# Kernel optimization log

Hardware: AMD Instinct MI355X
Metric: run time of the kernel (lower is better)

## Reference

```python
import jax, jax.numpy as jnp
import numpy as np

N = 50000      # nodes
K = 15         # k_max candidate neighbors per node
D = 128        # node_dim
H = 64         # hidden_dim
K_MIN = 2.0
K_MAX = 15.0
TAU = 0.5      # edge_tau
LAM = 1.0      # selector_lambda


def setup_inputs() -> dict:
    key = jax.random.key(0)
    ks = jax.random.split(key, 16)
    x = jax.random.normal(ks[0], (N, D), dtype=jnp.float32)
    src = jax.random.randint(ks[1], (N * K,), 0, N)
    dst = jnp.repeat(jnp.arange(N), K)  # edges grouped by dst, as the module requires
    edge_index = jnp.stack([src, dst]).astype(jnp.int64)
    edge_dist = jax.random.uniform(ks[2], (N * K,), dtype=jnp.float32)

    def lin(k, fin, fout):
        return jax.random.normal(k, (fin, fout), dtype=jnp.float32) / np.sqrt(fin)

    EIN = 2 * D + 1  # edge MLP input: [x_dst, x_src, dist]
    return {
        "x": x, "edge_index": edge_index, "edge_dist": edge_dist,
        "ew1": lin(ks[3], EIN, H), "eb1": jnp.zeros((H,), jnp.float32),
        "ew2": lin(ks[4], H, H),   "eb2": jnp.zeros((H,), jnp.float32),
        "ew3": lin(ks[5], H, 1),   "eb3": jnp.zeros((1,), jnp.float32),
        "dw1": lin(ks[6], D + 1, H), "db1": jnp.zeros((H,), jnp.float32),
        "dw2": lin(ks[7], H, H),     "db2": jnp.zeros((H,), jnp.float32),
        "dw3": lin(ks[8], H, 1),     "db3": jnp.zeros((1,), jnp.float32),
    }


def reference(x, edge_index, edge_dist, ew1, eb1, ew2, eb2, ew3, eb3,
              dw1, db1, dw2, db2, dw3, db3):
    src_mat = edge_index[0].reshape(N, K)              # (N, K)
    x_src = x[src_mat]                                 # gather: (N, K, D)
    x_dst = jnp.broadcast_to(x[:, None, :], (N, K, D))
    edge_feat = jnp.concatenate([x_dst, x_src, edge_dist.reshape(N, K, 1)], axis=-1)

    # edge MLP -> logits (eval mode: no gumbel-logistic noise)
    h = jax.nn.relu(edge_feat @ ew1 + eb1)
    h = jax.nn.relu(h @ ew2 + eb2)
    edge_logits = (h @ ew3 + eb3)[..., 0]              # (N, K)
    edge_energy = jax.nn.sigmoid(edge_logits / TAU)

    # degree MLP -> continuous k per node
    degree_hint = edge_energy.sum(axis=1, keepdims=True)
    g = jax.nn.relu(jnp.concatenate([x, degree_hint], axis=1) @ dw1 + db1)
    g = jax.nn.relu(g @ dw2 + db2)
    k_raw = (g @ dw3 + db3)[:, 0]
    k_cont = K_MIN + (K_MAX - K_MIN) * jax.nn.sigmoid(k_raw)  # (N,)

    # per-node descending sort + straight-through top-k gate
    perm = jnp.argsort(-edge_energy, axis=1)
    energy_sorted = jnp.take_along_axis(edge_energy, perm, axis=1)
    ranks = jnp.arange(1, K + 1, dtype=x.dtype)[None, :]
    gate_soft = jax.nn.sigmoid((k_cont[:, None] - ranks) / LAM)
    k_int = jnp.clip(jnp.round(k_cont), K_MIN, K_MAX)
    gate_hard = (ranks <= k_int[:, None]).astype(gate_soft.dtype)
    gate = gate_soft + jax.lax.stop_gradient(gate_hard - gate_soft)

    gated_sorted = energy_sorted * gate
    inv_perm = jnp.argsort(perm, axis=1)               # undo the sort
    edge_gate = jnp.take_along_axis(gate, inv_perm, axis=1)
    edge_weight = jnp.take_along_axis(gated_sorted, inv_perm, axis=1)

    denom = jnp.maximum(edge_weight.sum(axis=1, keepdims=True), 1e-12)
    edge_weight = edge_weight / denom
    return (edge_weight.reshape(-1), edge_gate.reshape(-1),
            edge_energy.reshape(-1), k_cont)
```

## Files before the change

kernel.cpp:

```cpp
#include <hip/hip_runtime.h>
#include <cmath>

#define NN 50000
#define KK 15
#define DD 128
#define HH 64
#define NKE (NN * KK)

__global__ __launch_bounds__(256) void kP(const float* __restrict__ x,
                                          const float* __restrict__ ew1,
                                          const float* __restrict__ dw1,
                                          float* __restrict__ ws) {
    int lane = threadIdx.x & 63;
    int wv = __builtin_amdgcn_readfirstlane((int)(threadIdx.x >> 6));
    int r0 = blockIdx.x * 32 + wv * 8;
    if (r0 >= NN) return;

    const float* W0 = ew1;
    const float* W1 = ew1 + DD * HH;
    const float* W2 = dw1;
    const float* xw = x + (size_t)r0 * DD;

    float a0[8], a1[8], a2[8];
#pragma unroll
    for (int r = 0; r < 8; ++r) { a0[r] = 0.f; a1[r] = 0.f; a2[r] = 0.f; }

#pragma unroll 1
    for (int i4 = 0; i4 < DD / 4; ++i4) {
        float w00 = W0[(i4 * 4 + 0) * HH + lane];
        float w01 = W0[(i4 * 4 + 1) * HH + lane];
        float w02 = W0[(i4 * 4 + 2) * HH + lane];
        float w03 = W0[(i4 * 4 + 3) * HH + lane];
        float w10 = W1[(i4 * 4 + 0) * HH + lane];
        float w11 = W1[(i4 * 4 + 1) * HH + lane];
        float w12 = W1[(i4 * 4 + 2) * HH + lane];
        float w13 = W1[(i4 * 4 + 3) * HH + lane];
        float w20 = W2[(i4 * 4 + 0) * HH + lane];
        float w21 = W2[(i4 * 4 + 1) * HH + lane];
        float w22 = W2[(i4 * 4 + 2) * HH + lane];
        float w23 = W2[(i4 * 4 + 3) * HH + lane];
#pragma unroll
        for (int r = 0; r < 8; ++r) {
            float4 xv = *(const float4*)(xw + r * DD + i4 * 4);
            a0[r] = fmaf(xv.x, w00, a0[r]);
            a0[r] = fmaf(xv.y, w01, a0[r]);
            a0[r] = fmaf(xv.z, w02, a0[r]);
            a0[r] = fmaf(xv.w, w03, a0[r]);
            a1[r] = fmaf(xv.x, w10, a1[r]);
            a1[r] = fmaf(xv.y, w11, a1[r]);
            a1[r] = fmaf(xv.z, w12, a1[r]);
            a1[r] = fmaf(xv.w, w13, a1[r]);
            a2[r] = fmaf(xv.x, w20, a2[r]);
            a2[r] = fmaf(xv.y, w21, a2[r]);
            a2[r] = fmaf(xv.z, w22, a2[r]);
            a2[r] = fmaf(xv.w, w23, a2[r]);
        }
    }
    float* o0 = ws + (size_t)r0 * HH + lane;
    float* o1 = ws + (size_t)NN * HH + (size_t)r0 * HH + lane;
    float* o2 = ws + 2 * (size_t)NN * HH + (size_t)r0 * HH + lane;
#pragma unroll
    for (int r = 0; r < 8; ++r) {
        o0[r * HH] = a0[r];
        o1[r * HH] = a1[r];
        o2[r * HH] = a2[r];
    }
}

__global__ __launch_bounds__(128, 4) void kE(const int* __restrict__ srcIdx,
                                             const float* __restrict__ dist,
                                             const float* __restrict__ ws,
                                             const float* __restrict__ ew1,
                                             const float* __restrict__ eb1,
                                             const float* __restrict__ ew2,
                                             const float* __restrict__ eb2,
                                             const float* __restrict__ ew3,
                                             const float* __restrict__ eb3,
                                             float* __restrict__ energy_out) {
    int lane = threadIdx.x & 63;
    int wv = __builtin_amdgcn_readfirstlane((int)(threadIdx.x >> 6));
    int e = blockIdx.x * 64 + lane;
    __shared__ float lred[2][64];

    bool valid = e < NKE;
    int ec = valid ? e : (NKE - 1);
    int s = srcIdx[ec];
    int d = ec / KK;
    float dd = dist[ec];
    const float* A = ws + (size_t)d * HH;
    const float* B = ws + (size_t)NN * HH + (size_t)s * HH;
    const float* w1l = ew1 + 2 * DD * HH;
    const float* W2  = ew2 + wv * 32;
    const float* eb2s = eb2 + wv * 32;
    const float* ew3s = ew3 + wv * 32;

    float acc[32];
#pragma unroll
    for (int j = 0; j < 32; ++j) acc[j] = 0.f;

    float4 a4 = *(const float4*)A;
    float4 b4 = *(const float4*)B;
#pragma unroll 1
    for (int i4 = 0; i4 < HH / 4; ++i4) {
        float4 a = a4, b = b4;
        int nx = (i4 + 1 < HH / 4) ? (i4 + 1) : i4;
        a4 = *(const float4*)(A + nx * 4);
        b4 = *(const float4*)(B + nx * 4);
        float h[4];
        h[0] = fmaxf(a.x + b.x + dd * w1l[i4 * 4 + 0] + eb1[i4 * 4 + 0], 0.f);
        h[1] = fmaxf(a.y + b.y + dd * w1l[i4 * 4 + 1] + eb1[i4 * 4 + 1], 0.f);
        h[2] = fmaxf(a.z + b.z + dd * w1l[i4 * 4 + 2] + eb1[i4 * 4 + 2], 0.f);
        h[3] = fmaxf(a.w + b.w + dd * w1l[i4 * 4 + 3] + eb1[i4 * 4 + 3], 0.f);
#pragma unroll
        for (int k = 0; k < 4; ++k) {
            const float* wr = W2 + (i4 * 4 + k) * HH;
#pragma unroll
            for (int j4 = 0; j4 < 8; ++j4) {
                float4 w = *(const float4*)(wr + j4 * 4);
                acc[j4 * 4 + 0] = fmaf(h[k], w.x, acc[j4 * 4 + 0]);
                acc[j4 * 4 + 1] = fmaf(h[k], w.y, acc[j4 * 4 + 1]);
                acc[j4 * 4 + 2] = fmaf(h[k], w.z, acc[j4 * 4 + 2]);
                acc[j4 * 4 + 3] = fmaf(h[k], w.w, acc[j4 * 4 + 3]);
            }
        }
    }
    float lg = 0.f;
#pragma unroll
    for (int j = 0; j < 32; ++j)
        lg = fmaf(fmaxf(acc[j] + eb2s[j], 0.f), ew3s[j], lg);

    lred[wv][lane] = lg;
    __syncthreads();
    if (wv == 0 && valid) {
        float t = lred[0][lane] + lred[1][lane] + eb3[0];
        energy_out[e] = 1.f / (1.f + expf(-2.f * t));
    }
}

__global__ __launch_bounds__(256, 2) void kF(const float* __restrict__ ws,
                                             const float* __restrict__ dw1,
                                             const float* __restrict__ db1,
                                             const float* __restrict__ dw2,
                                             const float* __restrict__ db2,
                                             const float* __restrict__ dw3,
                                             const float* __restrict__ db3,
                                             float* __restrict__ out) {
    int lane = threadIdx.x & 63;
    int wv = __builtin_amdgcn_readfirstlane((int)(threadIdx.x >> 6));
    int n = blockIdx.x * 64 + lane;
    __shared__ float kred[4][64];

    bool valid = n < NN;
    int nc = valid ? n : (NN - 1);
    const float* energy = out + 2 * (size_t)NKE;

    float ev[KK];
    float dh = 0.f;
#pragma unroll
    for (int j = 0; j < KK; ++j) {
        ev[j] = energy[(size_t)nc * KK + j];
        dh += ev[j];
    }

    const float* XC  = ws + 2 * (size_t)NN * HH + (size_t)nc * HH;
    const float* w1l = dw1 + DD * HH;
    const float* W2  = dw2 + wv * 16;
    const float* db2s = db2 + wv * 16;
    const float* dw3s = dw3 + wv * 16;

    float acc[16];
#pragma unroll
    for (int j = 0; j < 16; ++j) acc[j] = 0.f;

    float4 c4 = *(const float4*)XC;
#pragma unroll 1
    for (int i4 = 0; i4 < HH / 4; ++i4) {
        float4 c = c4;
        int nx = (i4 + 1 < HH / 4) ? (i4 + 1) : i4;
        c4 = *(const float4*)(XC + nx * 4);
        float cv[4] = {c.x, c.y, c.z, c.w};
#pragma unroll
        for (int m = 0; m < 4; ++m) {
            int k = i4 * 4 + m;
            float g = fmaxf(cv[m] + dh * w1l[k] + db1[k], 0.f);
            const float* wr = W2 + k * HH;
#pragma unroll
            for (int j4 = 0; j4 < 4; ++j4) {
                float4 w = *(const float4*)(wr + j4 * 4);
                acc[j4 * 4 + 0] = fmaf(g, w.x, acc[j4 * 4 + 0]);
                acc[j4 * 4 + 1] = fmaf(g, w.y, acc[j4 * 4 + 1]);
                acc[j4 * 4 + 2] = fmaf(g, w.z, acc[j4 * 4 + 2]);
                acc[j4 * 4 + 3] = fmaf(g, w.w, acc[j4 * 4 + 3]);
            }
        }
    }
    float kp_ = 0.f;
#pragma unroll
    for (int j = 0; j < 16; ++j)
        kp_ = fmaf(fmaxf(acc[j] + db2s[j], 0.f), dw3s[j], kp_);

    kred[wv][lane] = kp_;
    __syncthreads();
    float kraw = kred[0][lane] + kred[1][lane] + kred[2][lane] + kred[3][lane]
               + db3[0];
    if (!valid) return;

    float kcont = 2.f + 13.f / (1.f + expf(-kraw));
    if (wv == 3) out[3 * (size_t)NKE + n] = kcont;

    float se[16];
    int si[16];
#pragma unroll
    for (int j = 0; j < KK; ++j) { se[j] = ev[j]; si[j] = j; }
    se[15] = -1.f; si[15] = 15;

#pragma unroll
    for (int pp = 1; pp < 16; pp <<= 1) {
#pragma unroll
        for (int k = pp; k >= 1; k >>= 1) {
#pragma unroll
            for (int j = k & (pp - 1); j + k < 16; j += 2 * k) {
#pragma unroll
                for (int i = 0; i < k; ++i) {
                    int a = i + j, b = i + j + k;
                    if (b < 16 && (a / (2 * pp)) == (b / (2 * pp))) {
                        bool sw = (se[b] > se[a]) ||
                                  (se[b] == se[a] && si[b] < si[a]);
                        float ea = sw ? se[b] : se[a];
                        float eb = sw ? se[a] : se[b];
                        int ia = sw ? si[b] : si[a];
                        int ib = sw ? si[a] : si[b];
                        se[a] = ea; se[b] = eb; si[a] = ia; si[b] = ib;
                    }
                }
            }
        }
    }

    float kint = rintf(kcont);
    kint = fminf(fmaxf(kint, 2.f), 15.f);

    float wsrt[KK];
    float denom = 0.f;
#pragma unroll
    for (int r = 0; r < KK; ++r) {
        float sel = ((float)(r + 1) <= kint) ? 1.f : 0.f;
        float wvv = se[r] * sel;
        wsrt[r] = wvv;
        denom += wvv;
    }
    denom = fmaxf(denom, 1e-12f);

#pragma unroll
    for (int r = 0; r < KK; ++r) {
        if ((r & 3) == wv) {
            float sel = ((float)(r + 1) <= kint) ? 1.f : 0.f;
            int j0 = si[r];
            out[(size_t)NKE + (size_t)n * KK + j0] = sel;
            out[(size_t)n * KK + j0] = wsrt[r] / denom;
        }
    }
}

extern "C" void kernel_launch(void* const* d_in, const int* in_sizes, int n_in,
                              void* d_out, int out_size, void* d_ws, size_t ws_size,
                              hipStream_t stream) {
    const float* x   = (const float*)d_in[0];
    const int*   ei  = (const int*)d_in[1];
    const float* ed  = (const float*)d_in[2];
    const float* ew1 = (const float*)d_in[3];
    const float* eb1 = (const float*)d_in[4];
    const float* ew2 = (const float*)d_in[5];
    const float* eb2 = (const float*)d_in[6];
    const float* ew3 = (const float*)d_in[7];
    const float* eb3 = (const float*)d_in[8];
    const float* dw1 = (const float*)d_in[9];
    const float* db1 = (const float*)d_in[10];
    const float* dw2 = (const float*)d_in[11];
    const float* db2 = (const float*)d_in[12];
    const float* dw3 = (const float*)d_in[13];
    const float* db3 = (const float*)d_in[14];
    float* out = (float*)d_out;
    float* ws  = (float*)d_ws;

    hipLaunchKernelGGL(kP, dim3((NN + 31) / 32), dim3(256), 0, stream,
                       x, ew1, dw1, ws);
    hipLaunchKernelGGL(kE, dim3((NKE + 63) / 64), dim3(128), 0, stream,
                       ei, ed, ws, ew1, eb1, ew2, eb2, ew3, eb3,
                       out + 2 * (size_t)NKE);
    hipLaunchKernelGGL(kF, dim3((NN + 63) / 64), dim3(256), 0, stream,
                       ws, dw1, db1, dw2, db2, dw3, db3, out);
}
```

Measured before the change: 291.5 us.

## Stage x tiles in LDS for projection and compute full hidden per edge thread

The projection kernel now loads a 64-row tile of x into padded shared memory. Each wave computes 32 output columns for 64 rows, with one row per lane and uniform (scalar/broadcast) weight loads, replacing the previous layout where lanes mapped to output columns. The edge kernel now gives each thread one edge and all 64 hidden units, which removes the two-wave split, the shared-memory reduction and the barrier, and halves the redundant A/B gathers. In exchange the edge kernel holds 64 accumulators per thread, which raises register pressure and may lower occupancy.

```diff
diff --git a/kernel.cpp b/kernel.cpp
--- a/kernel.cpp
+++ b/kernel.cpp
@@ -7,63 +7,61 @@
 #define HH 64
 #define NKE (NN * KK)
 
-__global__ __launch_bounds__(256) void kP(const float* __restrict__ x,
-                                          const float* __restrict__ ew1,
-                                          const float* __restrict__ dw1,
-                                          float* __restrict__ ws) {
-    int lane = threadIdx.x & 63;
-    int wv = __builtin_amdgcn_readfirstlane((int)(threadIdx.x >> 6));
-    int r0 = blockIdx.x * 32 + wv * 8;
-    if (r0 >= NN) return;
-
-    const float* W0 = ew1;
-    const float* W1 = ew1 + DD * HH;
-    const float* W2 = dw1;
-    const float* xw = x + (size_t)r0 * DD;
-
-    float a0[8], a1[8], a2[8];
-#pragma unroll
-    for (int r = 0; r < 8; ++r) { a0[r] = 0.f; a1[r] = 0.f; a2[r] = 0.f; }
-
+#define TP_ROWS 64
+#define TP_STRIDE 129
+
+__global__ __launch_bounds__(384, 2) void kP(const float* __restrict__ x,
+                                             const float* __restrict__ ew1,
+                                             const float* __restrict__ dw1,
+                                             float* __restrict__ ws) {
+    __shared__ float xt[TP_ROWS * TP_STRIDE];
+    int t = threadIdx.x;
+    int lane = t & 63;
+    int w = __builtin_amdgcn_readfirstlane(t >> 6);
+    int seg = w >> 1;
+    int jh  = w & 1;
+    int row0 = blockIdx.x * TP_ROWS;
+
+    for (int i = t; i < TP_ROWS * DD / 4; i += 384) {
+        int r = (i * 4) / DD;
+        int c = (i * 4) % DD;
+        float4 v = make_float4(0.f, 0.f, 0.f, 0.f);
+        if (row0 + r < NN) v = *(const float4*)(x + (size_t)(row0 + r) * DD + c);
+        float* p = &xt[r * TP_STRIDE + c];
+        p[0] = v.x; p[1] = v.y; p[2] = v.z; p[3] = v.w;
+    }
+    __syncthreads();
+
+    const float* Wb = (seg == 0) ? (ew1 + jh * 32)
+                    : (seg == 1) ? (ew1 + (size_t)DD * HH + jh * 32)
+                                 : (dw1 + jh * 32);
+
+    float acc[32];
+#pragma unroll
+    for (int j = 0; j < 32; ++j) acc[j] = 0.f;
+
+    const float* xrow = &xt[lane * TP_STRIDE];
 #pragma unroll 1
-    for (int i4 = 0; i4 < DD / 4; ++i4) {
-        float w00 = W0[(i4 * 4 + 0) * HH + lane];
-        float w01 = W0[(i4 * 4 + 1) * HH + lane];
-        float w02 = W0[(i4 * 4 + 2) * HH + lane];
-        float w03 = W0[(i4 * 4 + 3) * HH + lane];
-        float w10 = W1[(i4 * 4 + 0) * HH + lane];
-        float w11 = W1[(i4 * 4 + 1) * HH + lane];
-        float w12 = W1[(i4 * 4 + 2) * HH + lane];
-        float w13 = W1[(i4 * 4 + 3) * HH + lane];
-        float w20 = W2[(i4 * 4 + 0) * HH + lane];
-        float w21 = W2[(i4 * 4 + 1) * HH + lane];
-        float w22 = W2[(i4 * 4 + 2) * HH + lane];
-        float w23 = W2[(i4 * 4 + 3) * HH + lane];
-#pragma unroll
-        for (int r = 0; r < 8; ++r) {
-            float4 xv = *(const float4*)(xw + r * DD + i4 * 4);
-            a0[r] = fmaf(xv.x, w00, a0[r]);
-            a0[r] = fmaf(xv.y, w01, a0[r]);
-            a0[r] = fmaf(xv.z, w02, a0[r]);
-            a0[r] = fmaf(xv.w, w03, a0[r]);
-            a1[r] = fmaf(xv.x, w10, a1[r]);
-            a1[r] = fmaf(xv.y, w11, a1[r]);
-            a1[r] = fmaf(xv.z, w12, a1[r]);
-            a1[r] = fmaf(xv.w, w13, a1[r]);
-            a2[r] = fmaf(xv.x, w20, a2[r]);
-            a2[r] = fmaf(xv.y, w21, a2[r]);
-            a2[r] = fmaf(xv.z, w22, a2[r]);
-            a2[r] = fmaf(xv.w, w23, a2[r]);
-        }
-    }
-    float* o0 = ws + (size_t)r0 * HH + lane;
-    float* o1 = ws + (size_t)NN * HH + (size_t)r0 * HH + lane;
-    float* o2 = ws + 2 * (size_t)NN * HH + (size_t)r0 * HH + lane;
-#pragma unroll
-    for (int r = 0; r < 8; ++r) {
-        o0[r * HH] = a0[r];
-        o1[r * HH] = a1[r];
-        o2[r * HH] = a2[r];
+    for (int k = 0; k < DD; ++k) {
+        float xv = xrow[k];
+        const float* wr = Wb + (size_t)k * HH;
+#pragma unroll
+        for (int j4 = 0; j4 < 8; ++j4) {
+            float4 wv = *(const float4*)(wr + j4 * 4);
+            acc[j4 * 4 + 0] = fmaf(xv, wv.x, acc[j4 * 4 + 0]);
+            acc[j4 * 4 + 1] = fmaf(xv, wv.y, acc[j4 * 4 + 1]);
+            acc[j4 * 4 + 2] = fmaf(xv, wv.z, acc[j4 * 4 + 2]);
+            acc[j4 * 4 + 3] = fmaf(xv, wv.w, acc[j4 * 4 + 3]);
+        }
+    }
+
+    int myrow = row0 + lane;
+    if (myrow < NN) {
+        float* o = ws + (size_t)seg * NN * HH + (size_t)myrow * HH + jh * 32;
+#pragma unroll
+        for (int j4 = 0; j4 < 8; ++j4)
+            *(float4*)(o + j4 * 4) = make_float4(acc[j4 * 4 + 0], acc[j4 * 4 + 1],
+                                                 acc[j4 * 4 + 2], acc[j4 * 4 + 3]);
     }
 }
 
@@ -77,26 +75,18 @@
                                              const float* __restrict__ ew3,
                                              const float* __restrict__ eb3,
                                              float* __restrict__ energy_out) {
-    int lane = threadIdx.x & 63;
-    int wv = __builtin_amdgcn_readfirstlane((int)(threadIdx.x >> 6));
-    int e = blockIdx.x * 64 + lane;
-    __shared__ float lred[2][64];
-
-    bool valid = e < NKE;
-    int ec = valid ? e : (NKE - 1);
-    int s = srcIdx[ec];
-    int d = ec / KK;
-    float dd = dist[ec];
+    int e = blockIdx.x * 128 + threadIdx.x;
+    if (e >= NKE) return;
+    int s = srcIdx[e];
+    int d = e / KK;
+    float dd = dist[e];
     const float* A = ws + (size_t)d * HH;
     const float* B = ws + (size_t)NN * HH + (size_t)s * HH;
     const float* w1l = ew1 + 2 * DD * HH;
-    const float* W2  = ew2 + wv * 32;
-    const float* eb2s = eb2 + wv * 32;
-    const float* ew3s = ew3 + wv * 32;
-
-    float acc[32];
-#pragma unroll
-    for (int j = 0; j < 32; ++j) acc[j] = 0.f;
+
+    float acc[HH];
+#pragma unroll
+    for (int j = 0; j < HH; ++j) acc[j] = 0.f;
 
     float4 a4 = *(const float4*)A;
     float4 b4 = *(const float4*)B;
@@ -113,9 +103,9 @@
         h[3] = fmaxf(a.w + b.w + dd * w1l[i4 * 4 + 3] + eb1[i4 * 4 + 3], 0.f);
 #pragma unroll
         for (int k = 0; k < 4; ++k) {
-            const float* wr = W2 + (i4 * 4 + k) * HH;
-#pragma unroll
-            for (int j4 = 0; j4 < 8; ++j4) {
+            const float* wr = ew2 + (i4 * 4 + k) * HH;
+#pragma unroll
+            for (int j4 = 0; j4 < 16; ++j4) {
                 float4 w = *(const float4*)(wr + j4 * 4);
                 acc[j4 * 4 + 0] = fmaf(h[k], w.x, acc[j4 * 4 + 0]);
                 acc[j4 * 4 + 1] = fmaf(h[k], w.y, acc[j4 * 4 + 1]);
@@ -124,17 +114,11 @@
             }
         }
     }
-    float lg = 0.f;
-#pragma unroll
-    for (int j = 0; j < 32; ++j)
-        lg = fmaf(fmaxf(acc[j] + eb2s[j], 0.f), ew3s[j], lg);
-
-    lred[wv][lane] = lg;
-    __syncthreads();
-    if (wv == 0 && valid) {
-        float t = lred[0][lane] + lred[1][lane] + eb3[0];
-        energy_out[e] = 1.f / (1.f + expf(-2.f * t));
-    }
+    float lg = eb3[0];
+#pragma unroll
+    for (int j = 0; j < HH; ++j)
+        lg = fmaf(fmaxf(acc[j] + eb2[j], 0.f), ew3[j], lg);
+    energy_out[e] = 1.f / (1.f + expf(-2.f * lg));
 }
 
 __global__ __launch_bounds__(256, 2) void kF(const float* __restrict__ ws,
@@ -283,9 +267,9 @@
     float* out = (float*)d_out;
     float* ws  = (float*)d_ws;
 
-    hipLaunchKernelGGL(kP, dim3((NN + 31) / 32), dim3(256), 0, stream,
+    hipLaunchKernelGGL(kP, dim3((NN + TP_ROWS - 1) / TP_ROWS), dim3(384), 0, stream,
                        x, ew1, dw1, ws);
-    hipLaunchKernelGGL(kE, dim3((NKE + 63) / 64), dim3(128), 0, stream,
+    hipLaunchKernelGGL(kE, dim3((NKE + 127) / 128), dim3(128), 0, stream,
                        ei, ed, ws, ew1, eb1, ew2, eb2, ew3, eb3,
                        out + 2 * (size_t)NKE);
     hipLaunchKernelGGL(kF, dim3((NN + 63) / 64), dim3(256), 0, stream,
```

Result: slower. 312.8 us (+7.3%).
